# Kernel tuning notes

Hardware: AMD Instinct MI355X
Metric: run time of the kernel (lower is better)

The kernel has to match this reference:

```python
import jax, jax.numpy as jnp
import numpy as np

B, N, K, NUM_CLASSES = 8, 4096, 16, 40
M = B * N


def _safe_norm(v):
    s = jnp.sum(v * v, axis=-1)
    return jnp.where(s > 0, jnp.sqrt(jnp.where(s > 0, s, 1.0)), 0.0)


def _angle(v1, v2):
    cn = _safe_norm(jnp.cross(v1, v2))
    d = jnp.sum(v1 * v2, axis=-1)
    ok = (cn > 0) | (d != 0)
    return jnp.where(ok, jnp.arctan2(cn, jnp.where(ok, d, 1.0)), 0.0)


def _ppf(pos_i, pos_j, n_i, n_j):
    # PyG point_pair_features: pseudo = pos_j - pos_i (j = source, i = target)
    pseudo = pos_j - pos_i
    return jnp.stack([_safe_norm(pseudo), _angle(n_i, pseudo),
                      _angle(n_j, pseudo), _angle(n_i, n_j)], axis=-1)


def _knn_edges(pos):
    # knn_graph(k=K, loop=False), per-graph; returns (src, dst) with self-loops
    # appended (PPFConv add_self_loops=True default).
    p = pos.reshape(B, N, 3)
    sq = jnp.sum(p * p, axis=-1)                                   # [B,N]
    d2 = sq[:, :, None] + sq[:, None, :] - 2.0 * jnp.einsum('bnd,bmd->bnm', p, p)
    d2 = jnp.where(jnp.eye(N, dtype=bool)[None], jnp.inf, d2)      # no loops
    _, nbr = jax.lax.top_k(-d2, K)                                  # [B,N,K]
    offs = (jnp.arange(B) * N)[:, None, None]
    src = (nbr + offs).reshape(-1)                                  # neighbors j
    dst = jnp.repeat(jnp.arange(M), K)                              # targets i
    loops = jnp.arange(M)
    return jnp.concatenate([src, loops]), jnp.concatenate([dst, loops])


def _mlp(e, w1, b1, w2, b2):
    return jax.nn.relu(e @ w1 + b1) @ w2 + b2


def setup_inputs() -> dict:
    key = jax.random.key(0)
    ks = jax.random.split(key, 12)
    pos = jax.random.normal(ks[0], (M, 3), jnp.float32)
    nrm = jax.random.normal(ks[1], (M, 3), jnp.float32)
    nrm = nrm / jnp.linalg.norm(nrm, axis=-1, keepdims=True)
    batch = jnp.repeat(jnp.arange(B, dtype=jnp.int32), N)
    s = 0.1
    return {
        'pos': pos, 'normal': nrm, 'batch': batch,
        'w1a': jax.random.normal(ks[2], (4, 32)) * s,  'b1a': jnp.zeros(32),
        'w1b': jax.random.normal(ks[3], (32, 32)) * s, 'b1b': jnp.zeros(32),
        'w2a': jax.random.normal(ks[4], (36, 32)) * s, 'b2a': jnp.zeros(32),
        'w2b': jax.random.normal(ks[5], (32, 32)) * s, 'b2b': jnp.zeros(32),
        'wc':  jax.random.normal(ks[6], (32, NUM_CLASSES)) * s,
        'bc':  jnp.zeros(NUM_CLASSES),
    }


def reference(pos, normal, batch, w1a, b1a, w1b, b1b, w2a, b2a, w2b, b2b, wc, bc):
    src, dst = _knn_edges(pos)
    feats = _ppf(pos[dst], pos[src], normal[dst], normal[src])      # [E,4]
    # conv1: x=None -> message = mlp1(ppf), scatter-max per target node
    msg1 = _mlp(feats, w1a, b1a, w1b, b1b)
    x = jax.nn.relu(jax.ops.segment_max(msg1, dst, num_segments=M))  # [M,32]
    # conv2: message = mlp2([x_j, ppf])
    msg2 = _mlp(jnp.concatenate([x[src], feats], axis=-1), w2a, b2a, w2b, b2b)
    x = jax.nn.relu(jax.ops.segment_max(msg2, dst, num_segments=M))
    # global_max_pool over each graph (uniform batch: reshape)
    g = x.reshape(B, N, 32).max(axis=1)                              # [B,32]
    return g @ wc + bc                                               # [B,40]
```

## Files before the change

kernel.cpp:

```cpp
#include <hip/hip_runtime.h>
#include <hip/hip_bf16.h>
#include <math.h>

#define NB 8
#define NN 4096
#define KK 16
#define MM (NB*NN)
#define CH 32
#define SLOTS 17
#define NCLS 40
#define BIG 3.0e38f
#define CAP 96
#define NBLK2 (MM/8)
#define HROW 36

#define OW1A 0
#define OB1A 128
#define OW1B 160
#define OB1B 1184
#define OW2A 1216
#define OB2A 2368
#define OW2B 2400
#define OB2B 3424
#define OWC  3456
#define OBC  4736
#define NWTS 4776

typedef short short8 __attribute__((ext_vector_type(8)));
typedef float f32x4  __attribute__((ext_vector_type(4)));

__device__ float4 g_pos4[MM];
__device__ float4 g_nrm4[MM];
__device__ int    g_nbr[MM*KK];
__device__ float  g_u[MM*CH];
__device__ float  g_bmax[NBLK2*CH];
__device__ float  g_wts[NWTS];
__device__ __align__(16) unsigned short g_wfrag1[2][2][64][8];
__device__ __align__(16) unsigned short g_wfrag2[2][2][64][8];

__device__ __forceinline__ float bf(const __hip_bfloat16 x) { return __bfloat162float(x); }

__device__ __forceinline__ float ldf(const void* p, int i, bool f32) {
  return f32 ? ((const float*)p)[i] : bf(((const __hip_bfloat16*)p)[i]);
}

__device__ __forceinline__ float angf(float ax, float ay, float az,
                                      float bx, float by, float bz) {
  float cx = ay*bz - az*by;
  float cy = az*bx - ax*bz;
  float cz = ax*by - ay*bx;
  float s  = cx*cx + cy*cy + cz*cz;
  float cn = s > 0.f ? sqrtf(s) : 0.f;
  float d  = ax*bx + ay*by + az*bz;
  return (cn > 0.f || d != 0.f) ? atan2f(cn, d) : 0.f;
}

__device__ __forceinline__ void ppf4(const float4 pi, const float4 ni,
                                     const float4 pj, const float4 nj, float* f) {
  float px = pj.x - pi.x, py = pj.y - pi.y, pz = pj.z - pi.z;
  float s = px*px + py*py + pz*pz;
  f[0] = s > 0.f ? sqrtf(s) : 0.f;
  f[1] = angf(ni.x, ni.y, ni.z, px, py, pz);
  f[2] = angf(nj.x, nj.y, nj.z, px, py, pz);
  f[3] = angf(ni.x, ni.y, ni.z, nj.x, nj.y, nj.z);
}

__device__ __forceinline__ unsigned int fkey(float f) {
  unsigned int u = __float_as_uint(f);
  return (u & 0x80000000u) ? ~u : (u | 0x80000000u);
}
__device__ __forceinline__ float funkey(unsigned int k) {
  unsigned int u = (k & 0x80000000u) ? (k ^ 0x80000000u) : ~k;
  return __uint_as_float(u);
}

__device__ __forceinline__ void bsplit(float v, unsigned short* hi, unsigned short* lo) {
  __hip_bfloat16 h = __float2bfloat16(v);
  float hf = __bfloat162float(h);
  __hip_bfloat16 l = __float2bfloat16(v - hf);
  *hi = *reinterpret_cast<unsigned short*>(&h);
  *lo = *reinterpret_cast<unsigned short*>(&l);
}

__device__ __forceinline__ void afrag(const float* row, short8* ah, short8* al) {
  float4 a = *(const float4*)row;
  float4 b = *(const float4*)(row + 4);
  unsigned short h, l;
  #pragma unroll
  for (int j = 0; j < 4; ++j) {
    bsplit((&a.x)[j], &h, &l); (*ah)[j]   = (short)h; (*al)[j]   = (short)l;
    bsplit((&b.x)[j], &h, &l); (*ah)[j+4] = (short)h; (*al)[j+4] = (short)l;
  }
}

__global__ __launch_bounds__(256) void prep_kernel(
    const void* __restrict__ pos, const void* __restrict__ nrm,
    const void* w1a, const void* b1a, const void* w1b, const void* b1b,
    const void* w2a, const void* b2a, const void* w2b, const void* b2b,
    const void* wc, const void* bc) {
  __shared__ int sflag;
  const int tid = threadIdx.x;
  const int base = blockIdx.x << 8;
  if (tid < 64) {
    const float* nf = (const float*)nrm;
    const __hip_bfloat16* nh = (const __hip_bfloat16*)nrm;
    int n = base + tid;
    float x = nf[3*n], y = nf[3*n+1], z = nf[3*n+2];
    float ss = x*x + y*y + z*z;
    bool okf = (ss > 0.98f && ss < 1.02f);
    float a = bf(nh[3*n]), b2 = bf(nh[3*n+1]), c2 = bf(nh[3*n+2]);
    float sb = a*a + b2*b2 + c2*c2;
    bool okb = (sb > 0.95f && sb < 1.05f);
    unsigned long long mf = __ballot(okf), mb = __ballot(okb);
    if (tid == 0) sflag = (__popcll(mf) >= __popcll(mb)) ? 1 : 0;
  }
  __syncthreads();
  const bool f32 = sflag != 0;
  {
    int i = base + tid;
    float x = ldf(pos, 3*i, f32), y = ldf(pos, 3*i+1, f32), z = ldf(pos, 3*i+2, f32);
    g_pos4[i] = make_float4(x, y, z, x*x + y*y + z*z);
    float a = ldf(nrm, 3*i, f32), bb = ldf(nrm, 3*i+1, f32), cc = ldf(nrm, 3*i+2, f32);
    g_nrm4[i] = make_float4(a, bb, cc, 0.f);
  }
  if (blockIdx.x == 0) {
    for (int t = tid; t < 128;  t += 256) g_wts[OW1A + t] = ldf(w1a, t, f32);
    for (int t = tid; t < 32;   t += 256) g_wts[OB1A + t] = ldf(b1a, t, f32);
    for (int t = tid; t < 1024; t += 256) g_wts[OW1B + t] = ldf(w1b, t, f32);
    for (int t = tid; t < 32;   t += 256) g_wts[OB1B + t] = ldf(b1b, t, f32);
    for (int t = tid; t < 1152; t += 256) g_wts[OW2A + t] = ldf(w2a, t, f32);
    for (int t = tid; t < 32;   t += 256) g_wts[OB2A + t] = ldf(b2a, t, f32);
    for (int t = tid; t < 1024; t += 256) g_wts[OW2B + t] = ldf(w2b, t, f32);
    for (int t = tid; t < 32;   t += 256) g_wts[OB2B + t] = ldf(b2b, t, f32);
    for (int t = tid; t < 1280; t += 256) g_wts[OWC  + t] = ldf(wc,  t, f32);
    for (int t = tid; t < 40;   t += 256) g_wts[OBC  + t] = ldf(bc,  t, f32);
    for (int t = tid; t < 4096; t += 256) {
      int which = t >> 11;
      int r = t & 2047;
      int tt = r >> 10;  r &= 1023;
      int hl = r >> 9;   r &= 511;
      int ln = r >> 3;
      int j  = r & 7;
      int k = (ln >> 4)*8 + j;
      int c = tt*16 + (ln & 15);
      float wv = ldf(which ? w2b : w1b, k*CH + c, f32);
      unsigned short hi, lo;
      bsplit(wv, &hi, &lo);
      unsigned short v = hl ? lo : hi;
      if (which) g_wfrag2[tt][hl][ln][j] = v;
      else       g_wfrag1[tt][hl][ln][j] = v;
    }
  }
}

__global__ __launch_bounds__(512) void knn_conv1_kernel() {
  __shared__ __align__(16) union SU {
    struct {
      float sx[NN], sy[NN], sz[NN];
      unsigned short ilst[64][CAP];
      double dlst[8][CAP];
    } k;
    struct {
      float fe[272][4];
      float h1s[288*HROW];
      float wsaT[32*HROW];
      float xs[16][CH];
    } c;
  } u;
  __shared__ unsigned short nbrs[64][KK];
  __shared__ unsigned short swcnt[64];

  const int tid  = threadIdx.x;
  const int w    = tid >> 6, lane = tid & 63;
  const int blk  = blockIdx.x;
  const int b    = blk >> 6;
  const int qbw  = ((blk & 63) << 6) | (w << 3);
  const float4* bp = g_pos4 + b*NN;

  #pragma unroll
  for (int k = 0; k < 8; ++k) {
    int idx = k*512 + tid;
    float4 o = bp[idx];
    u.k.sx[idx] = o.x; u.k.sy[idx] = o.y; u.k.sz[idx] = o.z;
  }
  __syncthreads();

  float q2x[8], q2y[8], q2z[8];
  #pragma unroll
  for (int qq = 0; qq < 8; ++qq) {
    int qi = qbw + qq;
    q2x[qq] = -2.f*u.k.sx[qi]; q2y[qq] = -2.f*u.k.sy[qi]; q2z[qq] = -2.f*u.k.sz[qi];
  }

  float mn[8];
  #pragma unroll
  for (int qq = 0; qq < 8; ++qq) mn[qq] = BIG;
  #pragma unroll 4
  for (int it = 0; it < 64; ++it) {
    int idx = it*64 + lane;
    float ox = u.k.sx[idx], oy = u.k.sy[idx], oz = u.k.sz[idx];
    float ow = __builtin_fmaf(oz, oz, __builtin_fmaf(oy, oy, ox*ox));
    #pragma unroll
    for (int qq = 0; qq < 8; ++qq) {
      float d = __builtin_fmaf(q2x[qq], ox,
                __builtin_fmaf(q2y[qq], oy,
                __builtin_fmaf(q2z[qq], oz, ow)));
      mn[qq] = fminf(mn[qq], d);
    }
  }

  unsigned int key[8], lo[8], hi[8];
  #pragma unroll
  for (int qq = 0; qq < 8; ++qq) { key[qq] = fkey(mn[qq]) >> 16; lo[qq] = 0u; hi[qq] = 0xFFFFu; }
  #pragma unroll 1
  for (int s = 0; s < 16; ++s) {
    #pragma unroll
    for (int qq = 0; qq < 8; ++qq) {
      unsigned int mid = (lo[qq] + hi[qq]) >> 1;
      int c = (int)__popcll(__ballot(key[qq] <= mid));
      if (c >= 17) hi[qq] = mid; else lo[qq] = mid + 1;
    }
  }
  float Tf[8];
  #pragma unroll
  for (int qq = 0; qq < 8; ++qq) {
    float T = funkey((hi[qq] << 16) | 0xFFFFu);
    Tf[qq] = T + 4e-5f + 1e-5f*fabsf(T);
  }

  unsigned int scnt[8];
  #pragma unroll
  for (int qq = 0; qq < 8; ++qq) scnt[qq] = 0u;
  #pragma unroll 4
  for (int it = 0; it < 64; ++it) {
    int idx = it*64 + lane;
    float ox = u.k.sx[idx], oy = u.k.sy[idx], oz = u.k.sz[idx];
    float ow = __builtin_fmaf(oz, oz, __builtin_fmaf(oy, oy, ox*ox));
    #pragma unroll
    for (int qq = 0; qq < 8; ++qq) {
      float d = __builtin_fmaf(q2x[qq], ox,
                __builtin_fmaf(q2y[qq], oy,
                __builtin_fmaf(q2z[qq], oz, ow)));
      unsigned long long mk = __ballot(d <= Tf[qq]);
      if (mk) {
        unsigned int cbase = scnt[qq];
        if (d <= Tf[qq]) {
          unsigned int r = __builtin_amdgcn_mbcnt_hi(
              (unsigned int)(mk >> 32),
              __builtin_amdgcn_mbcnt_lo((unsigned int)mk, 0u));
          unsigned int p = cbase + r;
          if (p < CAP) u.k.ilst[(w<<3)|qq][p] = (unsigned short)idx;
        }
        scnt[qq] = cbase + (unsigned int)__popcll(mk);
      }
    }
  }
  if (lane == 0) {
    #pragma unroll
    for (int qq = 0; qq < 8; ++qq)
      swcnt[(w<<3)|qq] = (unsigned short)min((int)scnt[qq], CAP);
  }

  #pragma unroll 1
  for (int qq = 0; qq < 8; ++qq) {
    const int qi = qbw + qq;
    const int ql = (w<<3) | qq;
    const int m = (int)swcnt[ql];
    const double mx = (double)u.k.sx[qi], my_ = (double)u.k.sy[qi], mz = (double)u.k.sz[qi];
    const double sqme = (mx*mx + my_*my_) + mz*mz;
    for (int e = lane; e < m; e += 64) {
      int ci = u.k.ilst[ql][e];
      double ox = (double)u.k.sx[ci], oy = (double)u.k.sy[ci], oz = (double)u.k.sz[ci];
      double sqo = (ox*ox + oy*oy) + oz*oz;
      double dt  = (mx*ox + my_*oy) + mz*oz;
      u.k.dlst[w][e] = (sqme + sqo) - 2.0*dt;
    }
    for (int e = lane; e < m; e += 64) {
      double myd = u.k.dlst[w][e];
      int myi = u.k.ilst[ql][e];
      int rank = 0;
      for (int o = 0; o < m; ++o) {
        double od = u.k.dlst[w][o];
        int oi = u.k.ilst[ql][o];
        rank += (od < myd) || (od == myd && oi < myi);
      }
      if (rank >= 1 && rank <= KK) {
        nbrs[ql][rank-1] = (unsigned short)myi;
        g_nbr[(b*NN + qi)*KK + (rank-1)] = b*NN + myi;
      }
    }
  }

  const int c32 = tid & 31;
  const int quad = lane >> 4, l15 = lane & 15;
  float w1a_c[4];
  #pragma unroll
  for (int f = 0; f < 4; ++f) w1a_c[f] = g_wts[OW1A + f*CH + c32];
  const float b1a_c = g_wts[OB1A + c32];
  short8 bH0 = *(const short8*)&g_wfrag1[0][0][lane][0];
  short8 bL0 = *(const short8*)&g_wfrag1[0][1][lane][0];
  short8 bH1 = *(const short8*)&g_wfrag1[1][0][lane][0];
  short8 bL1 = *(const short8*)&g_wfrag1[1][1][lane][0];
  const float bias0 = g_wts[OB1B + l15];
  const float bias1 = g_wts[OB1B + 16 + l15];

  __syncthreads();

  for (int i2 = tid; i2 < 1024; i2 += 512) {
    int k = i2 >> 5, cc = i2 & 31;
    u.c.wsaT[cc*HROW + k] = g_wts[OW2A + i2];
  }
  const int nbb = b*NN + ((blk & 63) << 6);

  #pragma unroll 1
  for (int ck = 0; ck < 4; ++ck) {
    const int nloc0 = ck << 4;
    if (tid < 272) {
      int ns = tid / 17, slot = tid - ns*17;
      int iloc = nloc0 + ns;
      int ig = nbb + iloc;
      int jg = (slot < KK) ? (b*NN + (int)nbrs[iloc][slot]) : ig;
      ppf4(g_pos4[ig], g_nrm4[ig], g_pos4[jg], g_nrm4[jg], u.c.fe[tid]);
    }
    __syncthreads();
    #pragma unroll
    for (int it = 0; it < 17; ++it) {
      int idx = it*512 + tid;
      int e = idx >> 5;
      float4 f4 = *(const float4*)u.c.fe[e];
      float h = b1a_c + f4.x*w1a_c[0] + f4.y*w1a_c[1] + f4.z*w1a_c[2] + f4.w*w1a_c[3];
      u.c.h1s[e*HROW + c32] = fmaxf(h, 0.f);
    }
    __syncthreads();
    #pragma unroll
    for (int ni = 0; ni < 2; ++ni) {
      const int n16 = w*2 + ni;
      const int rbase = n16*17;
      short8 ah0, al0, ah1, al1;
      afrag(&u.c.h1s[(rbase      + l15)*HROW + quad*8], &ah0, &al0);
      afrag(&u.c.h1s[(rbase + 16 + l15)*HROW + quad*8], &ah1, &al1);
      f32x4 a00 = {0.f,0.f,0.f,0.f}, a01 = a00, a10 = a00, a11 = a00;
      a00 = __builtin_amdgcn_mfma_f32_16x16x32_bf16(ah0, bH0, a00, 0, 0, 0);
      a00 = __builtin_amdgcn_mfma_f32_16x16x32_bf16(ah0, bL0, a00, 0, 0, 0);
      a00 = __builtin_amdgcn_mfma_f32_16x16x32_bf16(al0, bH0, a00, 0, 0, 0);
      a01 = __builtin_amdgcn_mfma_f32_16x16x32_bf16(ah0, bH1, a01, 0, 0, 0);
      a01 = __builtin_amdgcn_mfma_f32_16x16x32_bf16(ah0, bL1, a01, 0, 0, 0);
      a01 = __builtin_amdgcn_mfma_f32_16x16x32_bf16(al0, bH1, a01, 0, 0, 0);
      a10 = __builtin_amdgcn_mfma_f32_16x16x32_bf16(ah1, bH0, a10, 0, 0, 0);
      a10 = __builtin_amdgcn_mfma_f32_16x16x32_bf16(ah1, bL0, a10, 0, 0, 0);
      a10 = __builtin_amdgcn_mfma_f32_16x16x32_bf16(al1, bH0, a10, 0, 0, 0);
      a11 = __builtin_amdgcn_mfma_f32_16x16x32_bf16(ah1, bH1, a11, 0, 0, 0);
      a11 = __builtin_amdgcn_mfma_f32_16x16x32_bf16(ah1, bL1, a11, 0, 0, 0);
      a11 = __builtin_amdgcn_mfma_f32_16x16x32_bf16(al1, bH1, a11, 0, 0, 0);
      float m0 = fmaxf(fmaxf(a00[0], a00[1]), fmaxf(a00[2], a00[3]));
      float m1 = fmaxf(fmaxf(a01[0], a01[1]), fmaxf(a01[2], a01[3]));
      if (quad == 0) { m0 = fmaxf(m0, a10[0]); m1 = fmaxf(m1, a11[0]); }
      m0 = fmaxf(m0, __shfl_xor(m0, 16)); m0 = fmaxf(m0, __shfl_xor(m0, 32));
      m1 = fmaxf(m1, __shfl_xor(m1, 16)); m1 = fmaxf(m1, __shfl_xor(m1, 32));
      if (quad == 0) {
        u.c.xs[n16][l15]      = fmaxf(m0 + bias0, 0.f);
        u.c.xs[n16][16 + l15] = fmaxf(m1 + bias1, 0.f);
      }
    }
    __syncthreads();
    {
      int ns = tid >> 5;
      float uu = 0.f;
      #pragma unroll
      for (int k4 = 0; k4 < 8; ++k4) {
        float4 x4 = *(const float4*)&u.c.xs[ns][4*k4];
        float4 w4 = *(const float4*)&u.c.wsaT[c32*HROW + 4*k4];
        uu += x4.x*w4.x + x4.y*w4.y + x4.z*w4.z + x4.w*w4.w;
      }
      g_u[(nbb + nloc0 + ns)*CH + c32] = uu;
    }
    __syncthreads();
  }
}

__global__ __launch_bounds__(256) void conv2_kernel() {
  __shared__ __align__(16) float fe[136][4];
  __shared__ int jn[136];
  __shared__ __align__(16) float h1s[152*HROW];
  __shared__ float xs[8][CH];
  const int tid = threadIdx.x;
  const int c = tid & 31;
  const int lane = tid & 63, wv = tid >> 6;
  const int quad = lane >> 4, l15 = lane & 15;
  const int node0 = blockIdx.x << 3;
  float w2aL_c[4];
  #pragma unroll
  for (int f = 0; f < 4; ++f) w2aL_c[f] = g_wts[OW2A + (CH + f)*CH + c];
  const float b2a_c = g_wts[OB2A + c];
  short8 bH0 = *(const short8*)&g_wfrag2[0][0][lane][0];
  short8 bL0 = *(const short8*)&g_wfrag2[0][1][lane][0];
  short8 bH1 = *(const short8*)&g_wfrag2[1][0][lane][0];
  short8 bL1 = *(const short8*)&g_wfrag2[1][1][lane][0];
  const float bias0 = g_wts[OB2B + l15];
  const float bias1 = g_wts[OB2B + 16 + l15];

  if (tid < 136) {
    int ns = tid / 17, slot = tid - ns*17;
    int i = node0 + ns;
    int j = (slot < KK) ? g_nbr[i*KK + slot] : i;
    jn[tid] = j;
    ppf4(g_pos4[i], g_nrm4[i], g_pos4[j], g_nrm4[j], fe[tid]);
  }
  __syncthreads();
  #pragma unroll
  for (int it = 0; it < 17; ++it) {
    int idx = it*256 + tid;
    int e = idx >> 5;
    float4 f4 = *(const float4*)fe[e];
    float uv = g_u[jn[e]*CH + c];
    float h = b2a_c + uv + f4.x*w2aL_c[0] + f4.y*w2aL_c[1] + f4.z*w2aL_c[2] + f4.w*w2aL_c[3];
    h1s[e*HROW + c] = fmaxf(h, 0.f);
  }
  __syncthreads();
  #pragma unroll
  for (int ni = 0; ni < 2; ++ni) {
    const int n8 = wv*2 + ni;
    const int rbase = n8*17;
    short8 ah0, al0, ah1, al1;
    afrag(&h1s[(rbase      + l15)*HROW + quad*8], &ah0, &al0);
    afrag(&h1s[(rbase + 16 + l15)*HROW + quad*8], &ah1, &al1);
    f32x4 a00 = {0.f,0.f,0.f,0.f}, a01 = a00, a10 = a00, a11 = a00;
    a00 = __builtin_amdgcn_mfma_f32_16x16x32_bf16(ah0, bH0, a00, 0, 0, 0);
    a00 = __builtin_amdgcn_mfma_f32_16x16x32_bf16(ah0, bL0, a00, 0, 0, 0);
    a00 = __builtin_amdgcn_mfma_f32_16x16x32_bf16(al0, bH0, a00, 0, 0, 0);
    a01 = __builtin_amdgcn_mfma_f32_16x16x32_bf16(ah0, bH1, a01, 0, 0, 0);
    a01 = __builtin_amdgcn_mfma_f32_16x16x32_bf16(ah0, bL1, a01, 0, 0, 0);
    a01 = __builtin_amdgcn_mfma_f32_16x16x32_bf16(al0, bH1, a01, 0, 0, 0);
    a10 = __builtin_amdgcn_mfma_f32_16x16x32_bf16(ah1, bH0, a10, 0, 0, 0);
    a10 = __builtin_amdgcn_mfma_f32_16x16x32_bf16(ah1, bL0, a10, 0, 0, 0);
    a10 = __builtin_amdgcn_mfma_f32_16x16x32_bf16(al1, bH0, a10, 0, 0, 0);
    a11 = __builtin_amdgcn_mfma_f32_16x16x32_bf16(ah1, bH1, a11, 0, 0, 0);
    a11 = __builtin_amdgcn_mfma_f32_16x16x32_bf16(ah1, bL1, a11, 0, 0, 0);
    a11 = __builtin_amdgcn_mfma_f32_16x16x32_bf16(al1, bH1, a11, 0, 0, 0);
    float m0 = fmaxf(fmaxf(a00[0], a00[1]), fmaxf(a00[2], a00[3]));
    float m1 = fmaxf(fmaxf(a01[0], a01[1]), fmaxf(a01[2], a01[3]));
    if (quad == 0) { m0 = fmaxf(m0, a10[0]); m1 = fmaxf(m1, a11[0]); }
    m0 = fmaxf(m0, __shfl_xor(m0, 16)); m0 = fmaxf(m0, __shfl_xor(m0, 32));
    m1 = fmaxf(m1, __shfl_xor(m1, 16)); m1 = fmaxf(m1, __shfl_xor(m1, 32));
    if (quad == 0) {
      xs[n8][l15]      = fmaxf(m0 + bias0, 0.f);
      xs[n8][16 + l15] = fmaxf(m1 + bias1, 0.f);
    }
  }
  __syncthreads();
  if (tid < CH) {
    float m2 = xs[0][c];
    #pragma unroll
    for (int r = 1; r < 8; ++r) m2 = fmaxf(m2, xs[r][c]);
    g_bmax[blockIdx.x*CH + c] = m2;
  }
}

__global__ __launch_bounds__(256) void head_kernel(float* __restrict__ out) {
  __shared__ float red[8][CH];
  __shared__ float gm[CH];
  const int g = blockIdx.x;
  const int c = threadIdx.x & 31, sub = threadIdx.x >> 5;
  const float* base = g_bmax + (size_t)(g*512 + sub*64)*CH;
  float mx = 0.f;
  #pragma unroll
  for (int n = 0; n < 64; ++n) mx = fmaxf(mx, base[n*CH + c]);
  red[sub][c] = mx;
  __syncthreads();
  if (threadIdx.x < CH) {
    float m2 = red[0][c];
    #pragma unroll
    for (int r = 1; r < 8; ++r) m2 = fmaxf(m2, red[r][c]);
    gm[c] = m2;
  }
  __syncthreads();
  if (threadIdx.x < NCLS) {
    int co = threadIdx.x;
    float s = g_wts[OBC + co];
    #pragma unroll
    for (int f = 0; f < CH; ++f) s += gm[f] * g_wts[OWC + f*NCLS + co];
    out[g*NCLS + co] = s;
  }
}

extern "C" void kernel_launch(void* const* d_in, const int* in_sizes, int n_in,
                              void* d_out, int out_size, void* d_ws, size_t ws_size,
                              hipStream_t stream) {
  const void* pos = d_in[0];
  const void* nrm = d_in[1];
  const void* w1a = d_in[3];
  const void* b1a = d_in[4];
  const void* w1b = d_in[5];
  const void* b1b = d_in[6];
  const void* w2a = d_in[7];
  const void* b2a = d_in[8];
  const void* w2b = d_in[9];
  const void* b2b = d_in[10];
  const void* wc  = d_in[11];
  const void* bc  = d_in[12];

  prep_kernel<<<MM/256, 256, 0, stream>>>(pos, nrm, w1a, b1a, w1b, b1b,
                                          w2a, b2a, w2b, b2b, wc, bc);
  knn_conv1_kernel<<<MM/64, 512, 0, stream>>>();
  conv2_kernel<<<MM/8, 256, 0, stream>>>();
  head_kernel<<<NB, 256, 0, stream>>>((float*)d_out);
}
```

Before: 197.1 us.

## Cache PPF features from conv1 and enlarge conv2 blocks; pack kNN distance loop

conv1 now writes its point-pair features to a global buffer, and conv2 reads them back instead of recomputing the four atan2-based angles per edge. conv2 moves to 512-thread blocks that each handle 64 nodes in four chunks and keep a running per-block max, so there are fewer blocks and fewer g_bmax partials; the head kernel is adjusted to match. The kNN distance and threshold loops process two candidates per lane as float2 vectors with paired ballots. The cost is an extra feature buffer of about 9 MB written and read through global memory.

Measured after the change: 191.7 us. 1.03x faster.

```diff
diff --git a/kernel.cpp b/kernel.cpp
--- a/kernel.cpp
+++ b/kernel.cpp
@@ -11,7 +11,7 @@
 #define NCLS 40
 #define BIG 3.0e38f
 #define CAP 96
-#define NBLK2 (MM/8)
+#define NBLK2 (MM/64)
 #define HROW 36
 
 #define OW1A 0
@@ -28,6 +28,7 @@
 
 typedef short short8 __attribute__((ext_vector_type(8)));
 typedef float f32x4  __attribute__((ext_vector_type(4)));
+typedef float f32x2  __attribute__((ext_vector_type(2)));
 
 __device__ float4 g_pos4[MM];
 __device__ float4 g_nrm4[MM];
@@ -35,6 +36,7 @@
 __device__ float  g_u[MM*CH];
 __device__ float  g_bmax[NBLK2*CH];
 __device__ float  g_wts[NWTS];
+__device__ __align__(16) float4 g_fe4[MM*SLOTS];
 __device__ __align__(16) unsigned short g_wfrag1[2][2][64][8];
 __device__ __align__(16) unsigned short g_wfrag2[2][2][64][8];
 
@@ -72,6 +74,11 @@
 __device__ __forceinline__ float funkey(unsigned int k) {
   unsigned int u = (k & 0x80000000u) ? (k ^ 0x80000000u) : ~k;
   return __uint_as_float(u);
+}
+
+__device__ __forceinline__ unsigned int mbcnt64(unsigned long long m) {
+  return __builtin_amdgcn_mbcnt_hi((unsigned int)(m >> 32),
+         __builtin_amdgcn_mbcnt_lo((unsigned int)m, 0u));
 }
 
 __device__ __forceinline__ void bsplit(float v, unsigned short* hi, unsigned short* lo) {
@@ -191,21 +198,28 @@
     int qi = qbw + qq;
     q2x[qq] = -2.f*u.k.sx[qi]; q2y[qq] = -2.f*u.k.sy[qi]; q2z[qq] = -2.f*u.k.sz[qi];
   }
+  const f32x2* sx2 = (const f32x2*)u.k.sx;
+  const f32x2* sy2 = (const f32x2*)u.k.sy;
+  const f32x2* sz2 = (const f32x2*)u.k.sz;
 
   float mn[8];
   #pragma unroll
   for (int qq = 0; qq < 8; ++qq) mn[qq] = BIG;
   #pragma unroll 4
-  for (int it = 0; it < 64; ++it) {
-    int idx = it*64 + lane;
-    float ox = u.k.sx[idx], oy = u.k.sy[idx], oz = u.k.sz[idx];
-    float ow = __builtin_fmaf(oz, oz, __builtin_fmaf(oy, oy, ox*ox));
+  for (int it = 0; it < 32; ++it) {
+    int p = it*64 + lane;
+    f32x2 ox = sx2[p], oy = sy2[p], oz = sz2[p];
+    f32x2 ow = __builtin_elementwise_fma(oz, oz,
+               __builtin_elementwise_fma(oy, oy, ox*ox));
     #pragma unroll
     for (int qq = 0; qq < 8; ++qq) {
-      float d = __builtin_fmaf(q2x[qq], ox,
-                __builtin_fmaf(q2y[qq], oy,
-                __builtin_fmaf(q2z[qq], oz, ow)));
-      mn[qq] = fminf(mn[qq], d);
+      f32x2 qx = {q2x[qq], q2x[qq]};
+      f32x2 qy = {q2y[qq], q2y[qq]};
+      f32x2 qz = {q2z[qq], q2z[qq]};
+      f32x2 d = __builtin_elementwise_fma(qx, ox,
+                __builtin_elementwise_fma(qy, oy,
+                __builtin_elementwise_fma(qz, oz, ow)));
+      mn[qq] = fminf(fminf(d[0], d[1]), mn[qq]);
     }
   }
 
@@ -231,27 +245,36 @@
   unsigned int scnt[8];
   #pragma unroll
   for (int qq = 0; qq < 8; ++qq) scnt[qq] = 0u;
-  #pragma unroll 4
-  for (int it = 0; it < 64; ++it) {
-    int idx = it*64 + lane;
-    float ox = u.k.sx[idx], oy = u.k.sy[idx], oz = u.k.sz[idx];
-    float ow = __builtin_fmaf(oz, oz, __builtin_fmaf(oy, oy, ox*ox));
+  #pragma unroll 2
+  for (int it = 0; it < 32; ++it) {
+    int p = it*64 + lane;
+    f32x2 ox = sx2[p], oy = sy2[p], oz = sz2[p];
+    f32x2 ow = __builtin_elementwise_fma(oz, oz,
+               __builtin_elementwise_fma(oy, oy, ox*ox));
     #pragma unroll
     for (int qq = 0; qq < 8; ++qq) {
-      float d = __builtin_fmaf(q2x[qq], ox,
-                __builtin_fmaf(q2y[qq], oy,
-                __builtin_fmaf(q2z[qq], oz, ow)));
-      unsigned long long mk = __ballot(d <= Tf[qq]);
-      if (mk) {
+      f32x2 qx = {q2x[qq], q2x[qq]};
+      f32x2 qy = {q2y[qq], q2y[qq]};
+      f32x2 qz = {q2z[qq], q2z[qq]};
+      f32x2 d = __builtin_elementwise_fma(qx, ox,
+                __builtin_elementwise_fma(qy, oy,
+                __builtin_elementwise_fma(qz, oz, ow)));
+      bool h0 = d[0] <= Tf[qq];
+      bool h1 = d[1] <= Tf[qq];
+      unsigned long long mk0 = __ballot(h0);
+      unsigned long long mk1 = __ballot(h1);
+      if (mk0 | mk1) {
         unsigned int cbase = scnt[qq];
-        if (d <= Tf[qq]) {
-          unsigned int r = __builtin_amdgcn_mbcnt_hi(
-              (unsigned int)(mk >> 32),
-              __builtin_amdgcn_mbcnt_lo((unsigned int)mk, 0u));
-          unsigned int p = cbase + r;
-          if (p < CAP) u.k.ilst[(w<<3)|qq][p] = (unsigned short)idx;
+        if (h0) {
+          unsigned int pos = cbase + mbcnt64(mk0);
+          if (pos < CAP) u.k.ilst[(w<<3)|qq][pos] = (unsigned short)(2*p);
         }
-        scnt[qq] = cbase + (unsigned int)__popcll(mk);
+        cbase += (unsigned int)__popcll(mk0);
+        if (h1) {
+          unsigned int pos = cbase + mbcnt64(mk1);
+          if (pos < CAP) u.k.ilst[(w<<3)|qq][pos] = (unsigned short)(2*p + 1);
+        }
+        scnt[qq] = cbase + (unsigned int)__popcll(mk1);
       }
     }
   }
@@ -320,7 +343,11 @@
       int iloc = nloc0 + ns;
       int ig = nbb + iloc;
       int jg = (slot < KK) ? (b*NN + (int)nbrs[iloc][slot]) : ig;
-      ppf4(g_pos4[ig], g_nrm4[ig], g_pos4[jg], g_nrm4[jg], u.c.fe[tid]);
+      float f[4];
+      ppf4(g_pos4[ig], g_nrm4[ig], g_pos4[jg], g_nrm4[jg], f);
+      float4 fv = make_float4(f[0], f[1], f[2], f[3]);
+      *(float4*)u.c.fe[tid] = fv;
+      g_fe4[(size_t)(nbb + nloc0)*SLOTS + tid] = fv;
     }
     __syncthreads();
     #pragma unroll
@@ -378,16 +405,16 @@
   }
 }
 
-__global__ __launch_bounds__(256) void conv2_kernel() {
-  __shared__ __align__(16) float fe[136][4];
-  __shared__ int jn[136];
-  __shared__ __align__(16) float h1s[152*HROW];
-  __shared__ float xs[8][CH];
+__global__ __launch_bounds__(512) void conv2_kernel() {
+  __shared__ __align__(16) float fe[272][4];
+  __shared__ int jn[272];
+  __shared__ __align__(16) float h1s[288*HROW];
+  __shared__ float xs[16][CH];
   const int tid = threadIdx.x;
   const int c = tid & 31;
   const int lane = tid & 63, wv = tid >> 6;
   const int quad = lane >> 4, l15 = lane & 15;
-  const int node0 = blockIdx.x << 3;
+  const int node0 = blockIdx.x << 6;
   float w2aL_c[4];
   #pragma unroll
   for (int f = 0; f < 4; ++f) w2aL_c[f] = g_wts[OW2A + (CH + f)*CH + c];
@@ -398,62 +425,66 @@
   short8 bL1 = *(const short8*)&g_wfrag2[1][1][lane][0];
   const float bias0 = g_wts[OB2B + l15];
   const float bias1 = g_wts[OB2B + 16 + l15];
-
-  if (tid < 136) {
-    int ns = tid / 17, slot = tid - ns*17;
-    int i = node0 + ns;
-    int j = (slot < KK) ? g_nbr[i*KK + slot] : i;
-    jn[tid] = j;
-    ppf4(g_pos4[i], g_nrm4[i], g_pos4[j], g_nrm4[j], fe[tid]);
-  }
-  __syncthreads();
-  #pragma unroll
-  for (int it = 0; it < 17; ++it) {
-    int idx = it*256 + tid;
-    int e = idx >> 5;
-    float4 f4 = *(const float4*)fe[e];
-    float uv = g_u[jn[e]*CH + c];
-    float h = b2a_c + uv + f4.x*w2aL_c[0] + f4.y*w2aL_c[1] + f4.z*w2aL_c[2] + f4.w*w2aL_c[3];
-    h1s[e*HROW + c] = fmaxf(h, 0.f);
-  }
-  __syncthreads();
-  #pragma unroll
-  for (int ni = 0; ni < 2; ++ni) {
-    const int n8 = wv*2 + ni;
-    const int rbase = n8*17;
-    short8 ah0, al0, ah1, al1;
-    afrag(&h1s[(rbase      + l15)*HROW + quad*8], &ah0, &al0);
-    afrag(&h1s[(rbase + 16 + l15)*HROW + quad*8], &ah1, &al1);
-    f32x4 a00 = {0.f,0.f,0.f,0.f}, a01 = a00, a10 = a00, a11 = a00;
-    a00 = __builtin_amdgcn_mfma_f32_16x16x32_bf16(ah0, bH0, a00, 0, 0, 0);
-    a00 = __builtin_amdgcn_mfma_f32_16x16x32_bf16(ah0, bL0, a00, 0, 0, 0);
-    a00 = __builtin_amdgcn_mfma_f32_16x16x32_bf16(al0, bH0, a00, 0, 0, 0);
-    a01 = __builtin_amdgcn_mfma_f32_16x16x32_bf16(ah0, bH1, a01, 0, 0, 0);
-    a01 = __builtin_amdgcn_mfma_f32_16x16x32_bf16(ah0, bL1, a01, 0, 0, 0);
-    a01 = __builtin_amdgcn_mfma_f32_16x16x32_bf16(al0, bH1, a01, 0, 0, 0);
-    a10 = __builtin_amdgcn_mfma_f32_16x16x32_bf16(ah1, bH0, a10, 0, 0, 0);
-    a10 = __builtin_amdgcn_mfma_f32_16x16x32_bf16(ah1, bL0, a10, 0, 0, 0);
-    a10 = __builtin_amdgcn_mfma_f32_16x16x32_bf16(al1, bH0, a10, 0, 0, 0);
-    a11 = __builtin_amdgcn_mfma_f32_16x16x32_bf16(ah1, bH1, a11, 0, 0, 0);
-    a11 = __builtin_amdgcn_mfma_f32_16x16x32_bf16(ah1, bL1, a11, 0, 0, 0);
-    a11 = __builtin_amdgcn_mfma_f32_16x16x32_bf16(al1, bH1, a11, 0, 0, 0);
-    float m0 = fmaxf(fmaxf(a00[0], a00[1]), fmaxf(a00[2], a00[3]));
-    float m1 = fmaxf(fmaxf(a01[0], a01[1]), fmaxf(a01[2], a01[3]));
-    if (quad == 0) { m0 = fmaxf(m0, a10[0]); m1 = fmaxf(m1, a11[0]); }
-    m0 = fmaxf(m0, __shfl_xor(m0, 16)); m0 = fmaxf(m0, __shfl_xor(m0, 32));
-    m1 = fmaxf(m1, __shfl_xor(m1, 16)); m1 = fmaxf(m1, __shfl_xor(m1, 32));
-    if (quad == 0) {
-      xs[n8][l15]      = fmaxf(m0 + bias0, 0.f);
-      xs[n8][16 + l15] = fmaxf(m1 + bias1, 0.f);
-    }
-  }
-  __syncthreads();
-  if (tid < CH) {
-    float m2 = xs[0][c];
-    #pragma unroll
-    for (int r = 1; r < 8; ++r) m2 = fmaxf(m2, xs[r][c]);
-    g_bmax[blockIdx.x*CH + c] = m2;
-  }
+  float bmx = 0.f;
+
+  #pragma unroll 1
+  for (int ck = 0; ck < 4; ++ck) {
+    const int n0 = node0 + (ck << 4);
+    if (tid < 272) {
+      int ns = tid / 17, slot = tid - ns*17;
+      int i = n0 + ns;
+      jn[tid] = (slot < KK) ? g_nbr[i*KK + slot] : i;
+      *(float4*)fe[tid] = g_fe4[(size_t)n0*SLOTS + tid];
+    }
+    __syncthreads();
+    #pragma unroll
+    for (int it = 0; it < 17; ++it) {
+      int idx = it*512 + tid;
+      int e = idx >> 5;
+      float4 f4 = *(const float4*)fe[e];
+      float uv = g_u[jn[e]*CH + c];
+      float h = b2a_c + uv + f4.x*w2aL_c[0] + f4.y*w2aL_c[1] + f4.z*w2aL_c[2] + f4.w*w2aL_c[3];
+      h1s[e*HROW + c] = fmaxf(h, 0.f);
+    }
+    __syncthreads();
+    #pragma unroll
+    for (int ni = 0; ni < 2; ++ni) {
+      const int n16 = wv*2 + ni;
+      const int rbase = n16*17;
+      short8 ah0, al0, ah1, al1;
+      afrag(&h1s[(rbase      + l15)*HROW + quad*8], &ah0, &al0);
+      afrag(&h1s[(rbase + 16 + l15)*HROW + quad*8], &ah1, &al1);
+      f32x4 a00 = {0.f,0.f,0.f,0.f}, a01 = a00, a10 = a00, a11 = a00;
+      a00 = __builtin_amdgcn_mfma_f32_16x16x32_bf16(ah0, bH0, a00, 0, 0, 0);
+      a00 = __builtin_amdgcn_mfma_f32_16x16x32_bf16(ah0, bL0, a00, 0, 0, 0);
+      a00 = __builtin_amdgcn_mfma_f32_16x16x32_bf16(al0, bH0, a00, 0, 0, 0);
+      a01 = __builtin_amdgcn_mfma_f32_16x16x32_bf16(ah0, bH1, a01, 0, 0, 0);
+      a01 = __builtin_amdgcn_mfma_f32_16x16x32_bf16(ah0, bL1, a01, 0, 0, 0);
+      a01 = __builtin_amdgcn_mfma_f32_16x16x32_bf16(al0, bH1, a01, 0, 0, 0);
+      a10 = __builtin_amdgcn_mfma_f32_16x16x32_bf16(ah1, bH0, a10, 0, 0, 0);
+      a10 = __builtin_amdgcn_mfma_f32_16x16x32_bf16(ah1, bL0, a10, 0, 0, 0);
+      a10 = __builtin_amdgcn_mfma_f32_16x16x32_bf16(al1, bH0, a10, 0, 0, 0);
+      a11 = __builtin_amdgcn_mfma_f32_16x16x32_bf16(ah1, bH1, a11, 0, 0, 0);
+      a11 = __builtin_amdgcn_mfma_f32_16x16x32_bf16(ah1, bL1, a11, 0, 0, 0);
+      a11 = __builtin_amdgcn_mfma_f32_16x16x32_bf16(al1, bH1, a11, 0, 0, 0);
+      float m0 = fmaxf(fmaxf(a00[0], a00[1]), fmaxf(a00[2], a00[3]));
+      float m1 = fmaxf(fmaxf(a01[0], a01[1]), fmaxf(a01[2], a01[3]));
+      if (quad == 0) { m0 = fmaxf(m0, a10[0]); m1 = fmaxf(m1, a11[0]); }
+      m0 = fmaxf(m0, __shfl_xor(m0, 16)); m0 = fmaxf(m0, __shfl_xor(m0, 32));
+      m1 = fmaxf(m1, __shfl_xor(m1, 16)); m1 = fmaxf(m1, __shfl_xor(m1, 32));
+      if (quad == 0) {
+        xs[n16][l15]      = fmaxf(m0 + bias0, 0.f);
+        xs[n16][16 + l15] = fmaxf(m1 + bias1, 0.f);
+      }
+    }
+    __syncthreads();
+    if (tid < CH) {
+      #pragma unroll
+      for (int r = 0; r < 16; ++r) bmx = fmaxf(bmx, xs[r][c]);
+    }
+    __syncthreads();
+  }
+  if (tid < CH) g_bmax[blockIdx.x*CH + c] = bmx;
 }
 
 __global__ __launch_bounds__(256) void head_kernel(float* __restrict__ out) {
@@ -461,10 +492,10 @@
   __shared__ float gm[CH];
   const int g = blockIdx.x;
   const int c = threadIdx.x & 31, sub = threadIdx.x >> 5;
-  const float* base = g_bmax + (size_t)(g*512 + sub*64)*CH;
+  const float* base = g_bmax + (size_t)(g*64 + sub*8)*CH;
   float mx = 0.f;
   #pragma unroll
-  for (int n = 0; n < 64; ++n) mx = fmaxf(mx, base[n*CH + c]);
+  for (int n = 0; n < 8; ++n) mx = fmaxf(mx, base[n*CH + c]);
   red[sub][c] = mx;
   __syncthreads();
   if (threadIdx.x < CH) {
@@ -502,6 +533,6 @@
   prep_kernel<<<MM/256, 256, 0, stream>>>(pos, nrm, w1a, b1a, w1b, b1b,
                                           w2a, b2a, w2b, b2b, wc, bc);
   knn_conv1_kernel<<<MM/64, 512, 0, stream>>>();
-  conv2_kernel<<<MM/8, 256, 0, stream>>>();
+  conv2_kernel<<<MM/64, 512, 0, stream>>>();
   head_kernel<<<NB, 256, 0, stream>>>((float*)d_out);
 }
```
